# Optimization experiments

Hardware: AMD Instinct MI355X
Metric: run time of the kernel (lower is better)

The kernel has to match this reference:

```python
import jax, jax.numpy as jnp
import numpy as np

N, E, F, R, S = 20000, 320000, 64, 8, 10
AVG_NEIGH = 16.0


def setup_inputs() -> dict:
    key = jax.random.key(0)
    ks = jax.random.split(key, 16)
    inp = {
        "vectors": jax.random.normal(ks[0], (E, 3), jnp.float32),
        "node_feats": jax.random.normal(ks[1], (N, F, 4), jnp.float32),  # [N, F, 1(0e)+3(1o)]
        "node_specie": jax.random.randint(ks[2], (N,), 0, S),
        "radial_embedding": jax.random.normal(ks[3], (E, R), jnp.float32),
        "senders": jax.random.randint(ks[4], (E,), 0, N),
        "receivers": jax.random.randint(ks[5], (E,), 0, N),
        # residual FullyConnectedTensorProduct(feats, one-hot species 0e) == species-dep. linear per l
        "W_res_s": jax.random.normal(ks[6], (S, F, F), jnp.float32),
        "W_res_v": jax.random.normal(ks[7], (S, F, F), jnp.float32),
        # interaction block: input linear per l
        "W_in_s": jax.random.normal(ks[8], (F, F), jnp.float32),
        "W_in_v": jax.random.normal(ks[9], (F, F), jnp.float32),
        # radial MLP -> 5 CG tensor-product path weights per channel
        "mlp_w1": jax.random.normal(ks[10], (R, 64), jnp.float32),
        "mlp_w2": jax.random.normal(ks[11], (64, 5 * F), jnp.float32) / 8.0,
        # interaction block: output linear per l
        "W_out_s": jax.random.normal(ks[12], (F, F), jnp.float32),
        "W_out_v": jax.random.normal(ks[13], (F, F), jnp.float32),
        # symmetric product basis (correlation 3), species-dependent term weights
        "W_prod_s": jax.random.normal(ks[14], (S, 5, F), jnp.float32) * 0.3,
        "W_prod_v": jax.random.normal(ks[15], (S, 4, F), jnp.float32) * 0.3,
    }
    k2 = jax.random.split(jax.random.key(1), 3)
    inp["W_lin_s"] = jax.random.normal(k2[0], (F, F), jnp.float32)
    inp["W_lin_v"] = jax.random.normal(k2[1], (F, F), jnp.float32)
    inp["W_read"] = jax.random.normal(k2[2], (F, 1), jnp.float32)
    return inp


def _forward(vectors, node_feats, node_specie, radial_embedding, senders, receivers,
             W_res_s, W_res_v, W_in_s, W_in_v, mlp_w1, mlp_w2, W_out_s, W_out_v,
             W_prod_s, W_prod_v, W_lin_s, W_lin_v, W_read):
    inv_sf = 1.0 / jnp.sqrt(jnp.float32(F))
    s = node_feats[..., 0]          # [N,F]   0e channels
    v = node_feats[..., 1:]         # [N,F,3] 1o channels

    # --- residual connection: FCTP(feats, one-hot species 0e attrs) -> species-gated linear per l
    res_s = jnp.einsum('nf,ngf->ng', s, W_res_s[node_specie]) * inv_sf
    res_v = jnp.einsum('nfc,ngf->ngc', v, W_res_v[node_specie]) * inv_sf

    # --- InteractionBlock ---
    h_s = (s @ W_in_s) * inv_sf
    h_v = jnp.einsum('nfc,fg->ngc', v, W_in_v) * inv_sf

    # spherical harmonics up to max_ell=1: Y0 = 1, Y1 = unit edge vector
    r = jnp.sqrt(jnp.sum(vectors * vectors, -1) + 1e-12)
    Y1 = vectors / r[:, None]                                # [E,3]

    # radial MLP produces per-edge weights for the 5 CG paths:
    # (0e x Y0 -> 0e), (1o . Y1 -> 0e), (0e x Y1 -> 1o), (1o x Y0 -> 1o), (1o x Y1 -> 1o, cross)
    w = (jax.nn.silu(radial_embedding @ mlp_w1) @ mlp_w2).reshape(-1, 5, F)  # [E,5,F]

    ss = h_s[senders]                                        # [E,F]
    sv = h_v[senders]                                        # [E,F,3]
    dot = jnp.einsum('efc,ec->ef', sv, Y1)                   # [E,F]
    m_s = w[:, 0] * ss + w[:, 1] * dot                       # [E,F]
    m_v = (w[:, 2] * ss)[:, :, None] * Y1[:, None, :] \
        + w[:, 3][:, :, None] * sv \
        + w[:, 4][:, :, None] * jnp.cross(sv, Y1[:, None, :])  # [E,F,3]

    agg_s = jnp.zeros_like(h_s).at[receivers].add(m_s) / AVG_NEIGH
    agg_v = jnp.zeros_like(h_v).at[receivers].add(m_v) / AVG_NEIGH
    a_s = (agg_s @ W_out_s) * inv_sf
    a_v = jnp.einsum('nfc,fg->ngc', agg_v, W_out_v) * inv_sf

    # --- EquivariantProductBasisBlock: correlation-3 symmetric contraction, species-dependent ---
    vv = jnp.sum(a_v * a_v, -1)                              # [N,F] invariant |v|^2
    Wp = W_prod_s[node_specie]                               # [N,5,F]
    p_s = (Wp[:, 0] * a_s + Wp[:, 1] * a_s ** 2 + Wp[:, 2] * a_s ** 3
           + Wp[:, 3] * vv + Wp[:, 4] * a_s * vv)
    Wv = W_prod_v[node_specie]                               # [N,4,F]
    p_v = (Wv[:, 0] + Wv[:, 1] * a_s + Wv[:, 2] * a_s ** 2 + Wv[:, 3] * vv)[:, :, None] * a_v

    f_s = (p_s @ W_lin_s) * inv_sf + res_s
    f_v = jnp.einsum('nfc,fg->ngc', p_v, W_lin_v) * inv_sf + res_v

    # --- LinearReadoutBlock (output_irreps = 0e), 1 head ---
    node_out = ((f_s @ W_read) * inv_sf)[:, None, :]         # [N, heads=1, 1]
    new_feats = jnp.concatenate([f_s[..., None], f_v], axis=-1)  # [N,F,4]
    return node_out, new_feats


def reference(vectors, node_feats, node_specie, radial_embedding, senders, receivers,
              W_res_s, W_res_v, W_in_s, W_in_v, mlp_w1, mlp_w2, W_out_s, W_out_v,
              W_prod_s, W_prod_v, W_lin_s, W_lin_v, W_read):
    return _forward(vectors, node_feats, node_specie, radial_embedding, senders, receivers,
                    W_res_s, W_res_v, W_in_s, W_in_v, mlp_w1, mlp_w2, W_out_s, W_out_v,
                    W_prod_s, W_prod_v, W_lin_s, W_lin_v, W_read)
```

## Files before the change

kernel.cpp:

```cpp
#include <hip/hip_runtime.h>
#include <math.h>

#define NN 20000
#define NE 320000
#define NF (NN*64)
#define TB 16

typedef float v2f __attribute__((ext_vector_type(2)));

#if __has_builtin(__builtin_elementwise_fma)
#define PKFMA(a,b,c) __builtin_elementwise_fma(a,b,c)
#else
static __device__ __forceinline__ v2f PKFMA(v2f a, v2f b, v2f c){
  v2f r; r.x = fmaf(a.x,b.x,c.x); r.y = fmaf(a.y,b.y,c.y); return r;
}
#endif

__global__ __launch_bounds__(256) void k_transpose_res(
    const float* __restrict__ Ws, const float* __restrict__ Wv,
    float* __restrict__ Wst, float* __restrict__ Wvt)
{
  int i = blockIdx.x*256 + threadIdx.x;
  int spec = i >> 12;
  int g = (i >> 6) & 63;
  int f = i & 63;
  Wst[spec*4096 + f*64 + g] = Ws[i];
  Wvt[spec*4096 + f*64 + g] = Wv[i];
}

__global__ __launch_bounds__(256) void k_hist_rank(const int* __restrict__ receivers,
                                                   int* __restrict__ count,
                                                   int* __restrict__ rank)
{
  int e = blockIdx.x*256 + threadIdx.x;
  rank[e] = atomicAdd(&count[receivers[e]], 1);
}

__global__ __launch_bounds__(256) void k_scan(const int* __restrict__ count,
                                              int* __restrict__ offset)
{
  __shared__ int part[256];
  int t = threadIdx.x;
  const int PER = 79;
  int s = 0;
  for(int i=0;i<PER;++i){ int idx = t*PER+i; if(idx < NN) s += count[idx]; }
  part[t] = s;
  __syncthreads();
  for(int off=1; off<256; off<<=1){
    int v = (t>=off) ? part[t-off] : 0;
    __syncthreads();
    part[t] += v;
    __syncthreads();
  }
  int run = t ? part[t-1] : 0;
  for(int i=0;i<PER;++i){
    int idx = t*PER+i;
    if(idx < NN){ offset[idx] = run; run += count[idx]; }
  }
  if(t==255) offset[NN] = run;
}

__global__ __launch_bounds__(256) void k_scatter(
    const int* __restrict__ senders, const int* __restrict__ receivers,
    const float* __restrict__ vectors, const float* __restrict__ radial,
    const int* __restrict__ offset, const int* __restrict__ rank,
    float* __restrict__ rec)
{
  int e = blockIdx.x*256 + threadIdx.x;
  int r = receivers[e];
  int slot = offset[r] + rank[e];
  float vx = vectors[e*3], vy = vectors[e*3+1], vz = vectors[e*3+2];
  float rinv = rsqrtf(vx*vx + vy*vy + vz*vz + 1e-12f);
  float4 ra = *(const float4*)(radial + (size_t)e*8);
  float4 rb = *(const float4*)(radial + (size_t)e*8 + 4);
  float* rp = rec + (size_t)slot*16;
  float4 w0; w0.x = vx*rinv; w0.y = vy*rinv; w0.z = vz*rinv; w0.w = __int_as_float(senders[e]);
  float4 w3; w3.x = __int_as_float(r); w3.y = 0.f; w3.z = 0.f; w3.w = 0.f;
  *(float4*)(rp)      = w0;
  *(float4*)(rp + 4)  = ra;
  *(float4*)(rp + 8)  = rb;
  *(float4*)(rp + 12) = w3;
}

__global__ __launch_bounds__(256) void k_node_pre(
    const float* __restrict__ node_feats, const float* __restrict__ W_in_s,
    const float* __restrict__ W_in_v, float* __restrict__ h)
{
  __shared__ float sh[16][4][64];
  int wave = threadIdx.x >> 6, lane = threadIdx.x & 63;
  int nb = blockIdx.x*16 + wave*4;
  #pragma unroll
  for(int k=0;k<4;++k){
    int nd = wave*4 + k;
    float4 nf = *(const float4*)(node_feats + (size_t)((nb+k)*64 + lane)*4);
    sh[nd][0][lane]=nf.x; sh[nd][1][lane]=nf.y; sh[nd][2][lane]=nf.z; sh[nd][3][lane]=nf.w;
  }
  __syncthreads();
  float as[4]={0,0,0,0}, a0[4]={0,0,0,0}, a1[4]={0,0,0,0}, a2[4]={0,0,0,0};
  for(int f=0; f<64; ++f){
    float ws = W_in_s[f*64+lane], wv = W_in_v[f*64+lane];
    #pragma unroll
    for(int k=0;k<4;++k){
      int nd = wave*4 + k;
      as[k] = fmaf(sh[nd][0][f], ws, as[k]);
      a0[k] = fmaf(sh[nd][1][f], wv, a0[k]);
      a1[k] = fmaf(sh[nd][2][f], wv, a1[k]);
      a2[k] = fmaf(sh[nd][3][f], wv, a2[k]);
    }
  }
  #pragma unroll
  for(int k=0;k<4;++k){
    float4 o4; o4.x = as[k]*0.125f; o4.y = a0[k]*0.125f;
    o4.z = a1[k]*0.125f; o4.w = a2[k]*0.125f;
    *(float4*)(h + (size_t)((nb+k)*64 + lane)*4) = o4;
  }
}

__global__ __launch_bounds__(256) void k_edge(
    const float* __restrict__ rec,
    const float* __restrict__ mlp_w1, const float* __restrict__ mlp_w2,
    const float* __restrict__ h, float* __restrict__ agg)
{
  __shared__ float recS[4][256];
  __shared__ float hid[4][64][20];
  int wave = threadIdx.x >> 6, lane = threadIdx.x & 63;
  int e0 = (blockIdx.x*4 + wave)*TB;

  *(float4*)&recS[wave][lane*4] = *(const float4*)(rec + (size_t)e0*16 + lane*4);

  float wl[8];
  #pragma unroll
  for(int r=0;r<8;++r) wl[r] = mlp_w1[r*64+lane];

  #pragma unroll
  for(int t=0;t<TB;++t){
    float acc = 0.f;
    #pragma unroll
    for(int r=0;r<8;++r) acc = fmaf(recS[wave][t*16+4+r], wl[r], acc);
    hid[wave][lane][t] = acc / (1.f + __expf(-acc));
  }

  v2f wv[5][8];
  #pragma unroll
  for(int j=0;j<5;++j)
    #pragma unroll
    for(int tp=0;tp<8;++tp) wv[j][tp] = (v2f){0.f, 0.f};
  const float* w2p = mlp_w2 + lane;
  for(int hh=0; hh<64; ++hh){
    float b[5];
    #pragma unroll
    for(int j=0;j<5;++j) b[j] = w2p[hh*320 + j*64];
    v2f hv[8];
    #pragma unroll
    for(int tp=0;tp<8;++tp) hv[tp] = *(const v2f*)&hid[wave][hh][2*tp];
    #pragma unroll
    for(int j=0;j<5;++j){
      v2f bb = {b[j], b[j]};
      #pragma unroll
      for(int tp=0;tp<8;++tp) wv[j][tp] = PKFMA(bb, hv[tp], wv[j][tp]);
    }
  }

  float4 hv4[4];
  #pragma unroll
  for(int p=0;p<4;++p){
    int snd = __float_as_int(recS[wave][p*16+3]);
    hv4[p] = *(const float4*)(h + (size_t)(snd*64 + lane)*4);
  }

  float as_=0.f, av0=0.f, av1=0.f, av2=0.f;
  int cur = __float_as_int(recS[wave][12]);
  #pragma unroll
  for(int t=0;t<TB;++t){
    float4 hc = hv4[t&3];
    if(t+4 < TB){
      int snd = __float_as_int(recS[wave][(t+4)*16+3]);
      hv4[t&3] = *(const float4*)(h + (size_t)(snd*64 + lane)*4);
    }
    int rcv = __float_as_int(recS[wave][t*16+12]);
    if(rcv != cur){
      size_t ro = (size_t)cur*256 + lane;
      atomicAdd(&agg[ro],     as_);
      atomicAdd(&agg[ro+64],  av0);
      atomicAdd(&agg[ro+128], av1);
      atomicAdd(&agg[ro+192], av2);
      as_=0.f; av0=0.f; av1=0.f; av2=0.f;
      cur = rcv;
    }
    float y0=recS[wave][t*16], y1=recS[wave][t*16+1], y2=recS[wave][t*16+2];
    float ss=hc.x, sv0=hc.y, sv1=hc.z, sv2=hc.w;
    float dot = sv0*y0 + sv1*y1 + sv2*y2;
    float wt0 = wv[0][t>>1][t&1], wt1 = wv[1][t>>1][t&1];
    float wt2 = wv[2][t>>1][t&1], wt3 = wv[3][t>>1][t&1], wt4 = wv[4][t>>1][t&1];
    as_ += wt0*ss + wt1*dot;
    float w2s = wt2*ss;
    av0 += w2s*y0 + wt3*sv0 + wt4*(sv1*y2 - sv2*y1);
    av1 += w2s*y1 + wt3*sv1 + wt4*(sv2*y0 - sv0*y2);
    av2 += w2s*y2 + wt3*sv2 + wt4*(sv0*y1 - sv1*y0);
  }
  size_t ro = (size_t)cur*256 + lane;
  atomicAdd(&agg[ro],     as_);
  atomicAdd(&agg[ro+64],  av0);
  atomicAdd(&agg[ro+128], av1);
  atomicAdd(&agg[ro+192], av2);
}

__global__ __launch_bounds__(256) void k_node_post(
  const float* __restrict__ node_feats, const int* __restrict__ specie,
  const float* __restrict__ agg,
  const float* __restrict__ Wrst, const float* __restrict__ Wrvt,
  const float* __restrict__ W_out_s, const float* __restrict__ W_out_v,
  const float* __restrict__ W_prod_s, const float* __restrict__ W_prod_v,
  const float* __restrict__ W_lin_s, const float* __restrict__ W_lin_v,
  const float* __restrict__ W_read, float* __restrict__ out_node,
  float* __restrict__ out_feats)
{
  __shared__ float shA[16][4][64];
  __shared__ float shS[16][4][64];
  int wave = threadIdx.x >> 6, lane = threadIdx.x & 63;
  int nb = blockIdx.x*16 + wave*4;
  #pragma unroll
  for(int k=0;k<4;++k){
    int nd = wave*4 + k;
    size_t o = (size_t)(nb+k)*256 + lane;
    shA[nd][0][lane] = agg[o]      * (1.f/16.f);
    shA[nd][1][lane] = agg[o+64]   * (1.f/16.f);
    shA[nd][2][lane] = agg[o+128]  * (1.f/16.f);
    shA[nd][3][lane] = agg[o+192]  * (1.f/16.f);
    float4 nf = *(const float4*)(node_feats + (size_t)((nb+k)*64 + lane)*4);
    shS[nd][0][lane]=nf.x; shS[nd][1][lane]=nf.y; shS[nd][2][lane]=nf.z; shS[nd][3][lane]=nf.w;
  }
  int spec[4];
  #pragma unroll
  for(int k=0;k<4;++k) spec[k] = specie[nb+k];
  __syncthreads();
  float a_s[4]={0,0,0,0}, a0[4]={0,0,0,0}, a1[4]={0,0,0,0}, a2[4]={0,0,0,0};
  float r_s[4]={0,0,0,0}, r0[4]={0,0,0,0}, r1[4]={0,0,0,0}, r2[4]={0,0,0,0};
  for(int f=0; f<64; ++f){
    float wos = W_out_s[f*64+lane], wov = W_out_v[f*64+lane];
    #pragma unroll
    for(int k=0;k<4;++k){
      int nd = wave*4 + k;
      a_s[k] = fmaf(shA[nd][0][f], wos, a_s[k]);
      a0[k]  = fmaf(shA[nd][1][f], wov, a0[k]);
      a1[k]  = fmaf(shA[nd][2][f], wov, a1[k]);
      a2[k]  = fmaf(shA[nd][3][f], wov, a2[k]);
    }
    #pragma unroll
    for(int k=0;k<4;++k){
      int nd = wave*4 + k;
      float wrs = Wrst[spec[k]*4096 + f*64 + lane];
      float wrv = Wrvt[spec[k]*4096 + f*64 + lane];
      r_s[k] = fmaf(shS[nd][0][f], wrs, r_s[k]);
      r0[k]  = fmaf(shS[nd][1][f], wrv, r0[k]);
      r1[k]  = fmaf(shS[nd][2][f], wrv, r1[k]);
      r2[k]  = fmaf(shS[nd][3][f], wrv, r2[k]);
    }
  }
  __syncthreads();
  #pragma unroll
  for(int k=0;k<4;++k){
    int nd = wave*4 + k;
    float A_s = a_s[k]*0.125f, A0 = a0[k]*0.125f, A1 = a1[k]*0.125f, A2 = a2[k]*0.125f;
    float vv = A0*A0 + A1*A1 + A2*A2;
    float as2 = A_s*A_s;
    const float* Wp = W_prod_s + spec[k]*320;
    float p_s = Wp[lane]*A_s + Wp[64+lane]*as2 + Wp[128+lane]*as2*A_s
              + Wp[192+lane]*vv + Wp[256+lane]*A_s*vv;
    const float* Wq = W_prod_v + spec[k]*256;
    float coef = Wq[lane] + Wq[64+lane]*A_s + Wq[128+lane]*as2 + Wq[192+lane]*vv;
    shS[nd][0][lane] = p_s;
    shS[nd][1][lane] = coef*A0;
    shS[nd][2][lane] = coef*A1;
    shS[nd][3][lane] = coef*A2;
  }
  __syncthreads();
  float lfs[4]={0,0,0,0}, lf0[4]={0,0,0,0}, lf1[4]={0,0,0,0}, lf2[4]={0,0,0,0};
  for(int f=0; f<64; ++f){
    float wls = W_lin_s[f*64+lane], wlv = W_lin_v[f*64+lane];
    #pragma unroll
    for(int k=0;k<4;++k){
      int nd = wave*4 + k;
      lfs[k] = fmaf(shS[nd][0][f], wls, lfs[k]);
      lf0[k] = fmaf(shS[nd][1][f], wlv, lf0[k]);
      lf1[k] = fmaf(shS[nd][2][f], wlv, lf1[k]);
      lf2[k] = fmaf(shS[nd][3][f], wlv, lf2[k]);
    }
  }
  float wr = W_read[lane];
  #pragma unroll
  for(int k=0;k<4;++k){
    int n = nb + k;
    float FS = lfs[k]*0.125f + r_s[k]*0.125f;
    float F0 = lf0[k]*0.125f + r0[k]*0.125f;
    float F1 = lf1[k]*0.125f + r1[k]*0.125f;
    float F2 = lf2[k]*0.125f + r2[k]*0.125f;
    float x = FS * wr;
    #pragma unroll
    for(int off=32; off; off>>=1) x += __shfl_down(x, off);
    if(lane==0) out_node[n] = x*0.125f;
    float4 o4; o4.x=FS; o4.y=F0; o4.z=F1; o4.w=F2;
    *(float4*)(out_feats + (size_t)(n*64+lane)*4) = o4;
  }
}

extern "C" void kernel_launch(void* const* d_in, const int* in_sizes, int n_in,
                              void* d_out, int out_size, void* d_ws, size_t ws_size,
                              hipStream_t stream) {
  const float* vectors    = (const float*)d_in[0];
  const float* node_feats = (const float*)d_in[1];
  const int*   node_specie= (const int*)  d_in[2];
  const float* radial     = (const float*)d_in[3];
  const int*   senders    = (const int*)  d_in[4];
  const int*   receivers  = (const int*)  d_in[5];
  const float* W_res_s    = (const float*)d_in[6];
  const float* W_res_v    = (const float*)d_in[7];
  const float* W_in_s     = (const float*)d_in[8];
  const float* W_in_v     = (const float*)d_in[9];
  const float* mlp_w1     = (const float*)d_in[10];
  const float* mlp_w2     = (const float*)d_in[11];
  const float* W_out_s    = (const float*)d_in[12];
  const float* W_out_v    = (const float*)d_in[13];
  const float* W_prod_s   = (const float*)d_in[14];
  const float* W_prod_v   = (const float*)d_in[15];
  const float* W_lin_s    = (const float*)d_in[16];
  const float* W_lin_v    = (const float*)d_in[17];
  const float* W_read     = (const float*)d_in[18];

  float* ws   = (float*)d_ws;
  float* h    = ws;
  float* agg  = ws + 4*(size_t)NF;
  float* Wrst = ws + 8*(size_t)NF;
  float* Wrvt = Wrst + 40960;
  float* rec  = Wrvt + 40960;
  int*   rank   = (int*)(rec + 16*(size_t)NE);
  int*   offset = rank + NE;
  int*   count  = offset + NN + 1;

  hipMemsetAsync(agg,   0, (size_t)4*NF*sizeof(float), stream);
  hipMemsetAsync(count, 0, (size_t)NN*sizeof(int), stream);
  k_transpose_res<<<160, 256, 0, stream>>>(W_res_s, W_res_v, Wrst, Wrvt);
  k_hist_rank<<<NE/256, 256, 0, stream>>>(receivers, count, rank);
  k_scan     <<<1,      256, 0, stream>>>(count, offset);
  k_scatter  <<<NE/256, 256, 0, stream>>>(senders, receivers, vectors, radial,
                                          offset, rank, rec);
  k_node_pre<<<NN/16, 256, 0, stream>>>(node_feats, W_in_s, W_in_v, h);
  k_edge<<<NE/(4*TB), 256, 0, stream>>>(rec, mlp_w1, mlp_w2, h, agg);
  k_node_post<<<NN/16, 256, 0, stream>>>(node_feats, node_specie, agg,
                                         Wrst, Wrvt, W_out_s, W_out_v,
                                         W_prod_s, W_prod_v, W_lin_s, W_lin_v,
                                         W_read, (float*)d_out, (float*)d_out + NN);
}
```

Measured before the change: 483.8 us.

## Stage MLP second-layer weights in LDS, fuse weight transpose into histogram, widen scan

The edge kernel now loads mlp_w2 cooperatively into shared memory in four 16-row chunks and reads it from there, instead of each lane issuing global loads per hidden unit. The inner loop is unrolled over two hidden rows at a time. The residual weight transpose is merged into the histogram/rank kernel to save a launch, and the single-block scan now uses 1024 threads with counts cached in registers. The edge kernel adds 20KB of LDS and extra block barriers, which may reduce occupancy.

```diff
diff --git a/kernel.cpp b/kernel.cpp
--- a/kernel.cpp
+++ b/kernel.cpp
@@ -16,48 +16,54 @@
 }
 #endif
 
-__global__ __launch_bounds__(256) void k_transpose_res(
+__global__ __launch_bounds__(256) void k_hist_prep(
+    const int* __restrict__ receivers, int* __restrict__ count, int* __restrict__ rank,
     const float* __restrict__ Ws, const float* __restrict__ Wv,
     float* __restrict__ Wst, float* __restrict__ Wvt)
 {
-  int i = blockIdx.x*256 + threadIdx.x;
-  int spec = i >> 12;
-  int g = (i >> 6) & 63;
-  int f = i & 63;
-  Wst[spec*4096 + f*64 + g] = Ws[i];
-  Wvt[spec*4096 + f*64 + g] = Wv[i];
-}
-
-__global__ __launch_bounds__(256) void k_hist_rank(const int* __restrict__ receivers,
-                                                   int* __restrict__ count,
-                                                   int* __restrict__ rank)
-{
   int e = blockIdx.x*256 + threadIdx.x;
   rank[e] = atomicAdd(&count[receivers[e]], 1);
-}
-
-__global__ __launch_bounds__(256) void k_scan(const int* __restrict__ count,
-                                              int* __restrict__ offset)
-{
-  __shared__ int part[256];
+  if(blockIdx.x < 160){
+    int i = blockIdx.x*256 + threadIdx.x;
+    int spec = i >> 12;
+    int g = (i >> 6) & 63;
+    int f = i & 63;
+    Wst[spec*4096 + f*64 + g] = Ws[i];
+    Wvt[spec*4096 + f*64 + g] = Wv[i];
+  }
+}
+
+__global__ __launch_bounds__(1024) void k_scan(const int* __restrict__ count,
+                                               int* __restrict__ offset)
+{
+  __shared__ int part[1024];
   int t = threadIdx.x;
-  const int PER = 79;
+  const int PER = 20;
+  int base = t*PER;
+  int loc[PER];
   int s = 0;
-  for(int i=0;i<PER;++i){ int idx = t*PER+i; if(idx < NN) s += count[idx]; }
+  #pragma unroll
+  for(int i=0;i<PER;++i){
+    int idx = base+i;
+    int v = (idx < NN) ? count[idx] : 0;
+    loc[i] = v; s += v;
+  }
   part[t] = s;
   __syncthreads();
-  for(int off=1; off<256; off<<=1){
+  for(int off=1; off<1024; off<<=1){
     int v = (t>=off) ? part[t-off] : 0;
     __syncthreads();
     part[t] += v;
     __syncthreads();
   }
   int run = t ? part[t-1] : 0;
+  #pragma unroll
   for(int i=0;i<PER;++i){
-    int idx = t*PER+i;
-    if(idx < NN){ offset[idx] = run; run += count[idx]; }
-  }
-  if(t==255) offset[NN] = run;
+    int idx = base+i;
+    if(idx < NN) offset[idx] = run;
+    run += loc[i];
+  }
+  if(t==1023) offset[NN] = part[1023];
 }
 
 __global__ __launch_bounds__(256) void k_scatter(
@@ -123,7 +129,9 @@
 {
   __shared__ float recS[4][256];
   __shared__ float hid[4][64][20];
-  int wave = threadIdx.x >> 6, lane = threadIdx.x & 63;
+  __shared__ float w2S[16*320];
+  int tid = threadIdx.x;
+  int wave = tid >> 6, lane = tid & 63;
   int e0 = (blockIdx.x*4 + wave)*TB;
 
   *(float4*)&recS[wave][lane*4] = *(const float4*)(rec + (size_t)e0*16 + lane*4);
@@ -145,19 +153,37 @@
   for(int j=0;j<5;++j)
     #pragma unroll
     for(int tp=0;tp<8;++tp) wv[j][tp] = (v2f){0.f, 0.f};
-  const float* w2p = mlp_w2 + lane;
-  for(int hh=0; hh<64; ++hh){
-    float b[5];
-    #pragma unroll
-    for(int j=0;j<5;++j) b[j] = w2p[hh*320 + j*64];
-    v2f hv[8];
-    #pragma unroll
-    for(int tp=0;tp<8;++tp) hv[tp] = *(const v2f*)&hid[wave][hh][2*tp];
-    #pragma unroll
-    for(int j=0;j<5;++j){
-      v2f bb = {b[j], b[j]};
+
+  for(int c=0;c<4;++c){
+    __syncthreads();
+    const float* src = mlp_w2 + c*16*320;
+    #pragma unroll
+    for(int k=0;k<5;++k){
+      int f4 = tid + k*256;
+      *(float4*)&w2S[f4*4] = *(const float4*)(src + (size_t)f4*4);
+    }
+    __syncthreads();
+    #pragma unroll
+    for(int hl=0; hl<16; hl+=2){
+      int hh = c*16 + hl;
+      float b0[5], b1[5];
       #pragma unroll
-      for(int tp=0;tp<8;++tp) wv[j][tp] = PKFMA(bb, hv[tp], wv[j][tp]);
+      for(int j=0;j<5;++j){
+        b0[j] = w2S[hl*320     + j*64 + lane];
+        b1[j] = w2S[(hl+1)*320 + j*64 + lane];
+      }
+      #pragma unroll
+      for(int tp=0;tp<8;++tp){
+        v2f h0 = *(const v2f*)&hid[wave][hh][2*tp];
+        v2f h1 = *(const v2f*)&hid[wave][hh+1][2*tp];
+        #pragma unroll
+        for(int j=0;j<5;++j){
+          v2f bb0 = {b0[j], b0[j]};
+          v2f bb1 = {b1[j], b1[j]};
+          wv[j][tp] = PKFMA(bb0, h0, wv[j][tp]);
+          wv[j][tp] = PKFMA(bb1, h1, wv[j][tp]);
+        }
+      }
     }
   }
 
@@ -339,13 +365,13 @@
 
   hipMemsetAsync(agg,   0, (size_t)4*NF*sizeof(float), stream);
   hipMemsetAsync(count, 0, (size_t)NN*sizeof(int), stream);
-  k_transpose_res<<<160, 256, 0, stream>>>(W_res_s, W_res_v, Wrst, Wrvt);
-  k_hist_rank<<<NE/256, 256, 0, stream>>>(receivers, count, rank);
-  k_scan     <<<1,      256, 0, stream>>>(count, offset);
+  k_hist_prep<<<NE/256, 256, 0, stream>>>(receivers, count, rank,
+                                          W_res_s, W_res_v, Wrst, Wrvt);
+  k_scan     <<<1,     1024, 0, stream>>>(count, offset);
   k_scatter  <<<NE/256, 256, 0, stream>>>(senders, receivers, vectors, radial,
                                           offset, rank, rec);
   k_node_pre<<<NN/16, 256, 0, stream>>>(node_feats, W_in_s, W_in_v, h);
-  k_edge<<<NE/(4*TB), 256, 0, stream>>>(rec, mlp_w1, mlp_w2, h, agg);
+  k_edge<<<NE/64, 256, 0, stream>>>(rec, mlp_w1, mlp_w2, h, agg);
   k_node_post<<<NN/16, 256, 0, stream>>>(node_feats, node_specie, agg,
                                          Wrst, Wrvt, W_out_s, W_out_v,
                                          W_prod_s, W_prod_v, W_lin_s, W_lin_v,
```

Result: faster. 458.8 us (-5.2%).
